# Kernel tuning notes

Hardware: AMD Instinct MI355X
Metric: run time of the kernel (lower is better)

Reference implementation:

```python
import jax, jax.numpy as jnp
import numpy as np

B, S, D, H = 4, 2048, 1024, 16
DK = D // H
THETA = 10000.0


def setup_inputs() -> dict:
    key = jax.random.key(0)
    ks = jax.random.split(key, 5)
    std = (1.0 / D) ** 0.5
    return {
        "x": jax.random.normal(ks[0], (B, S, D), dtype=jnp.float32),
        "q_proj": jax.random.normal(ks[1], (D, D), dtype=jnp.float32) * std,
        "k_proj": jax.random.normal(ks[2], (D, D), dtype=jnp.float32) * std,
        "v_proj": jax.random.normal(ks[3], (D, D), dtype=jnp.float32) * std,
        "o_proj": jax.random.normal(ks[4], (D, D), dtype=jnp.float32) * std,
        "token_positions": jnp.broadcast_to(jnp.arange(S, dtype=jnp.int32), (B, S)),
    }


def _apply_rope(t, cos, sin):
    # t: (B,H,S,DK); cos/sin: (B,1,S,DK//2). Interleaved even/odd rotation.
    even = t[..., 0::2]
    odd = t[..., 1::2]
    r_even = even * cos - odd * sin
    r_odd = even * sin + odd * cos
    return jnp.stack([r_even, r_odd], axis=-1).reshape(t.shape)


def reference(x, q_proj, k_proj, v_proj, o_proj, token_positions):
    b, s, d = x.shape
    # QKV projections: weights stored (out, in) -> x @ W^T
    q = (x @ q_proj.T).reshape(b, s, H, DK).transpose(0, 2, 1, 3)  # (B,H,S,DK)
    k = (x @ k_proj.T).reshape(b, s, H, DK).transpose(0, 2, 1, 3)
    v = (x @ v_proj.T).reshape(b, s, H, DK).transpose(0, 2, 1, 3)

    # RoPE angles from token positions
    inv_freq = 1.0 / (THETA ** (jnp.arange(0, DK, 2, dtype=jnp.float32) / DK))  # (DK/2,)
    ang = token_positions.astype(jnp.float32)[..., None] * inv_freq  # (B,S,DK/2)
    cos = jnp.cos(ang)[:, None, :, :]  # (B,1,S,DK/2)
    sin = jnp.sin(ang)[:, None, :, :]
    q = _apply_rope(q, cos, sin)
    k = _apply_rope(k, cos, sin)

    # Full causal attention with explicit score matrix (faithful to source)
    scores = jnp.einsum("bhqd,bhkd->bhqk", q, k) / (DK ** 0.5)
    causal = jnp.tril(jnp.ones((s, s), dtype=bool))
    scores = jnp.where(causal, scores, -jnp.inf)
    attn = jax.nn.softmax(scores, axis=-1)
    out = jnp.einsum("bhqk,bhkd->bhqd", attn, v)  # (B,H,S,DK)
    out = out.transpose(0, 2, 1, 3).reshape(b, s, d)  # (B,S,D)
    # o_proj stored (d_out, d_model): out @ o_proj^T
    return out @ o_proj.T
```

## Files before the change

### kernel.cpp

```cpp
#include <hip/hip_runtime.h>
#include <hip/hip_bf16.h>

using bf16x8 = __attribute__((ext_vector_type(8))) short;
using f32x4  = __attribute__((ext_vector_type(4))) float;

#define MFMA_BF16(a, b, c) __builtin_amdgcn_mfma_f32_16x16x32_bf16((a), (b), (c), 0, 0, 0)

__device__ __forceinline__ unsigned short f2bf(float x) {
  union { float f; unsigned int u; } v; v.f = x;
  unsigned int r = v.u + 0x7fffu + ((v.u >> 16) & 1u);
  return (unsigned short)(r >> 16);
}

__device__ __forceinline__ unsigned int cvtpk(float a, float b) {
  __hip_bfloat162 h = __float22bfloat162_rn(make_float2(a, b));
  unsigned int u; __builtin_memcpy(&u, &h, 4); return u;
}

__device__ __forceinline__ unsigned int pack_trunc(float a, float b) {
  unsigned int ua, ub;
  __builtin_memcpy(&ua, &a, 4);
  __builtin_memcpy(&ub, &b, 4);
  return (ua >> 16) | (ub & 0xFFFF0000u);
}

__device__ __forceinline__ float fast_exp2(float x) {
#if __has_builtin(__builtin_amdgcn_exp2f)
  return __builtin_amdgcn_exp2f(x);
#else
  return exp2f(x);
#endif
}

__device__ __forceinline__ void gload16(const void* g, void* l) {
  __builtin_amdgcn_global_load_lds(
      (const __attribute__((address_space(1))) unsigned int*)g,
      (__attribute__((address_space(3))) unsigned int*)l, 16, 0, 0);
}

__device__ __forceinline__ void wait_and_barrier() {
  asm volatile("s_waitcnt vmcnt(0)" ::: "memory");
  __builtin_amdgcn_sched_barrier(0);
  __builtin_amdgcn_s_barrier();
  __builtin_amdgcn_sched_barrier(0);
}

__global__ __launch_bounds__(256) void cvt_all(const float* __restrict__ x,
                                               const float* __restrict__ qw,
                                               const float* __restrict__ kw,
                                               const float* __restrict__ vw,
                                               const float* __restrict__ ow,
                                               unsigned short* __restrict__ out) {
  const int bid = blockIdx.x;
  int seg, loc;
  if (bid < 8192) { seg = 0; loc = bid; }
  else { seg = 1 + ((bid - 8192) >> 10); loc = (bid - 8192) & 1023; }
  const float* srcs[5] = {x, qw, kw, vw, ow};
  const float* in = srcs[seg];
  const size_t obase = (seg == 0) ? 0 : ((size_t)8192 + (size_t)(seg - 1) * 1024) * 1024;
  const int i = loc * 1024 + threadIdx.x * 4;
  float4 f = *(const float4*)(in + i);
  ushort4 o;
  o.x = f2bf(f.x); o.y = f2bf(f.y); o.z = f2bf(f.z); o.w = f2bf(f.w);
  *(ushort4*)(out + obase + i) = o;
}

__global__ __launch_bounds__(256) void rope_tab_k(const int* __restrict__ pos,
                                                  float2* __restrict__ tab) {
  const int row = blockIdx.x * 8 + (threadIdx.x >> 5);
  const int i = threadIdx.x & 31;
  const float p = (float)pos[row];
  const float invf = exp2f((float)(2 * i) * (-13.287712379549609f / 64.0f));
  float sn, cs;
  sincosf(p * invf, &sn, &cs);
  tab[(size_t)row * 32 + i] = make_float2(cs, sn);
}

template <int MODE>
__global__ __launch_bounds__(256) void gemm_bt(const unsigned short* __restrict__ A,
                                               const unsigned short* __restrict__ Bw,
                                               void* __restrict__ outp,
                                               const float2* __restrict__ tab,
                                               float oscale) {
  constexpr int K = 1024;
  __shared__ __align__(16) unsigned short smem[12288];
  const int tid  = threadIdx.x;
  const int lane = tid & 63, wave = tid >> 6;
  const int wr = wave >> 1, wc = wave & 1;
  const int bid = blockIdx.x + (blockIdx.y << 3);
  const int xcd = bid & 7;
  const int t6  = bid >> 3;
  const int bn0 = (t6 & 7) * 128;
  const int bm0 = (((t6 >> 3) << 3) + xcd) * 64;
  const int lrow = lane & 15, hi = lane >> 4, lko = hi * 8;
  const int srow = tid >> 2, scol = (tid & 3) * 8;
  const unsigned short* gA = A + (size_t)(bm0 + srow) * K + scol;
  const unsigned short* gB = Bw + (size_t)(bn0 + srow) * K + scol;
  const f32x4 z = {0.f, 0.f, 0.f, 0.f};
  f32x4 acc[2][4];
#pragma unroll
  for (int i = 0; i < 2; ++i)
#pragma unroll
    for (int j = 0; j < 4; ++j) acc[i][j] = z;

  auto stage = [&](int k0, int c) {
    char* base = (char*)smem + c * 12288;
    gload16(gA + k0, base + wave * 1024);
    gload16(gB + k0, base + 4096 + wave * 1024);
    gload16(gB + k0 + (size_t)64 * K, base + 8192 + wave * 1024);
  };

  stage(0, 0);
  int cur = 0;
#pragma unroll 1
  for (int k0 = 0; k0 < K; k0 += 32) {
    wait_and_barrier();
    if (k0 + 32 < K) stage(k0 + 32, cur ^ 1);
    const int ub = cur * 6144;
    bf16x8 af[2], bfr[4];
#pragma unroll
    for (int mi = 0; mi < 2; ++mi)
      af[mi] = *(const bf16x8*)&smem[ub + (wr * 32 + mi * 16 + lrow) * 32 + lko];
#pragma unroll
    for (int ni = 0; ni < 4; ++ni)
      bfr[ni] = *(const bf16x8*)&smem[ub + 2048 + (wc * 64 + ni * 16 + lrow) * 32 + lko];
#pragma unroll
    for (int mi = 0; mi < 2; ++mi)
#pragma unroll
      for (int ni = 0; ni < 4; ++ni)
        acc[mi][ni] = MFMA_BF16(af[mi], bfr[ni], acc[mi][ni]);
    cur ^= 1;
  }

  if (MODE == 2) {
#pragma unroll
    for (int mi = 0; mi < 2; ++mi)
#pragma unroll
      for (int r = 0; r < 4; ++r) {
        const int row = bm0 + wr * 32 + mi * 16 + hi * 4 + r;
#pragma unroll
        for (int ni = 0; ni < 4; ++ni) {
          const int col = bn0 + wc * 64 + ni * 16 + lrow;
          ((float*)outp)[(size_t)row * 1024 + col] = acc[mi][ni][r];
        }
      }
    return;
  }

  const int h0 = bn0 >> 6;
  const int bb = bm0 >> 11, s0 = bm0 & 2047;
  unsigned short* dst = (unsigned short*)outp;
  __syncthreads();
  if (MODE == 0) {
#pragma unroll
    for (int mi = 0; mi < 2; ++mi)
#pragma unroll
      for (int ni = 0; ni < 4; ++ni) {
        const int col = wc * 64 + ni * 16 + lrow;
        const int d = col & 63;
#pragma unroll
        for (int r = 0; r < 4; ++r) {
          const int row = wr * 32 + mi * 16 + hi * 4 + r;
          const float2 t = tab[(size_t)(bm0 + row) * 32 + (d >> 1)];
          const float v = acc[mi][ni][r];
          const float other = __shfl_xor(v, 1);
          const float rv = (d & 1) ? (other * t.y + v * t.x) : (v * t.x - other * t.y);
          smem[row * 136 + col] = f2bf(rv * oscale);
        }
      }
    __syncthreads();
#pragma unroll
    for (int it = 0; it < 4; ++it) {
      const int c = it * 256 + tid;
      const int hl = c >> 9, rem = c & 511;
      const int sl = rem >> 3, ch = (rem & 7) * 8;
      const bf16x8 val = *(const bf16x8*)&smem[sl * 136 + hl * 64 + ch];
      *(bf16x8*)&dst[((size_t)(bb * 16 + h0 + hl) * 2048 + s0 + sl) * 64 + ch] = val;
    }
  } else {
#pragma unroll
    for (int mi = 0; mi < 2; ++mi)
#pragma unroll
      for (int ni = 0; ni < 4; ++ni) {
        const int col = wc * 64 + ni * 16 + lrow;
        ushort4 pk;
        pk.x = f2bf(acc[mi][ni][0]); pk.y = f2bf(acc[mi][ni][1]);
        pk.z = f2bf(acc[mi][ni][2]); pk.w = f2bf(acc[mi][ni][3]);
        *(ushort4*)&smem[col * 72 + wr * 32 + mi * 16 + hi * 4] = pk;
      }
    __syncthreads();
#pragma unroll
    for (int it = 0; it < 4; ++it) {
      const int c = it * 256 + tid;
      const int cl = c >> 3, sc = (c & 7) * 8;
      const bf16x8 val = *(const bf16x8*)&smem[cl * 72 + sc];
      *(bf16x8*)&dst[((size_t)(bb * 16 + h0 + (cl >> 6)) * 64 + (cl & 63)) * 2048 + s0 + sc] = val;
    }
  }
}

__global__ __launch_bounds__(256) void attn_fwd(const unsigned short* __restrict__ Q,
                                                const unsigned short* __restrict__ Kk,
                                                const unsigned short* __restrict__ Vt,
                                                unsigned short* __restrict__ O) {
  __shared__ __align__(16) unsigned short Ks[8192];
  __shared__ __align__(16) unsigned short Vs[8192];
  __shared__ __align__(16) unsigned short Plds[4][16][64];
  const int p = blockIdx.x;
  const int L = (p & 7) * 128 + (p >> 3);
  const int bh = L >> 4, pair = L & 15;
  const int tid = threadIdx.x;
  const int lane = tid & 63, wave = tid >> 6;
  const int lrow = lane & 15, hi = lane >> 4;
  const int l7 = lrow & 7;
  const unsigned short* Qb = Q + (size_t)bh * 2048 * 64;
  const unsigned short* Kb = Kk + (size_t)bh * 2048 * 64;
  const unsigned short* Vb = Vt + (size_t)bh * 64 * 2048;
  const int rK   = tid >> 3;
  const int colK = ((tid & 7) ^ ((tid >> 3) & 7)) * 8;
  const int rV   = tid >> 4;
  const int colV = ((tid & 8) | ((tid & 7) ^ ((tid >> 4) & 7))) * 8;
  const int b = bh >> 4, h = bh & 15;
  const f32x4 z = {0.f, 0.f, 0.f, 0.f};
  const short one = (short)0x3F80;
  const bf16x8 ones = {one, one, one, one, one, one, one, one};

  auto stage128 = [&](int kv0) {
#pragma unroll
    for (int pass = 0; pass < 4; ++pass)
      gload16(Kb + (size_t)(kv0 + rK + 32 * pass) * 64 + colK,
              (char*)Ks + pass * 4096 + wave * 1024);
#pragma unroll
    for (int pass = 0; pass < 4; ++pass)
      gload16(Vb + (size_t)(rV + 16 * pass) * 2048 + kv0 + colV,
              (char*)Vs + pass * 4096 + wave * 1024);
  };
  auto stage64 = [&](int kv0) {
#pragma unroll
    for (int pass = 0; pass < 2; ++pass)
      gload16(Kb + (size_t)(kv0 + rK + 32 * pass) * 64 + colK,
              (char*)Ks + pass * 4096 + wave * 1024);
#pragma unroll
    for (int pass = 0; pass < 2; ++pass)
      gload16(Vb + (size_t)(rK + 32 * pass) * 2048 + kv0 + colK,
              (char*)Vs + pass * 4096 + wave * 1024);
  };

  for (int half = 0; half < 2; ++half) {
    const int qb = half ? (31 - pair) : pair;
    const int qrow = qb * 64 + wave * 16;
    const int qg = qrow + lrow;
    const bf16x8 qf0 = *(const bf16x8*)(Qb + (size_t)qg * 64 + hi * 8);
    const bf16x8 qf1 = *(const bf16x8*)(Qb + (size_t)qg * 64 + 32 + hi * 8);
    f32x4 acc[4] = {z, z, z, z};
    f32x4 acc_l = z;

    auto compute64 = [&](const char* Kbase, const char* Vbase, int vstride,
                         int kv0g, bool diag) {
      f32x4 st[4];
      __builtin_amdgcn_s_setprio(1);
#pragma unroll
      for (int n = 0; n < 4; ++n) {
        const int rk = n * 16 + lrow;
        const bf16x8 kf0 = *(const bf16x8*)(Kbase + rk * 128 + ((hi ^ l7) * 16));
        const bf16x8 kf1 = *(const bf16x8*)(Kbase + rk * 128 + (((4 + hi) ^ l7) * 16));
        st[n] = MFMA_BF16(kf0, qf0, z);
        st[n] = MFMA_BF16(kf1, qf1, st[n]);
      }
      __builtin_amdgcn_s_setprio(0);
      if (diag) {
#pragma unroll
        for (int n = 0; n < 4; ++n)
#pragma unroll
          for (int r = 0; r < 4; ++r)
            if (kv0g + n * 16 + hi * 4 + r > qg) st[n][r] = -1e30f;
      }
      float pe[16];
#pragma unroll
      for (int n = 0; n < 4; ++n)
#pragma unroll
        for (int r = 0; r < 4; ++r) pe[n * 4 + r] = fast_exp2(st[n][r]);
#pragma unroll
      for (int n = 0; n < 4; ++n) {
        uint2 pk;
        pk.x = pack_trunc(pe[n * 4 + 0], pe[n * 4 + 1]);
        pk.y = pack_trunc(pe[n * 4 + 2], pe[n * 4 + 3]);
        const int eo = ((((n * 2 + (hi >> 1)) ^ l7) << 3) | ((hi & 1) << 2));
        *(uint2*)&Plds[wave][lrow][eo] = pk;
      }
      const bf16x8 pf0 = *(const bf16x8*)&Plds[wave][lrow][(hi ^ l7) << 3];
      const bf16x8 pf1 = *(const bf16x8*)&Plds[wave][lrow][((4 + hi) ^ l7) << 3];
      __builtin_amdgcn_s_setprio(1);
      acc_l = MFMA_BF16(ones, pf0, acc_l);
      acc_l = MFMA_BF16(ones, pf1, acc_l);
#pragma unroll
      for (int dt = 0; dt < 4; ++dt) {
        const int rv = dt * 16 + lrow;
        const bf16x8 vf0 = *(const bf16x8*)(Vbase + rv * vstride + ((hi ^ l7) * 16));
        const bf16x8 vf1 = *(const bf16x8*)(Vbase + rv * vstride + (((4 + hi) ^ l7) * 16));
        acc[dt] = MFMA_BF16(vf0, pf0, acc[dt]);
        acc[dt] = MFMA_BF16(vf1, pf1, acc[dt]);
      }
      __builtin_amdgcn_s_setprio(0);
    };

    const int F = (qb + 1) >> 1;
    const bool tail = ((qb & 1) == 0);
#pragma unroll 1
    for (int f = 0; f < F; ++f) {
      const int kv0 = f * 128;
      __syncthreads();
      stage128(kv0);
      __syncthreads();
      compute64((char*)Ks, (char*)Vs, 256, kv0, false);
      compute64((char*)Ks + 8192, (char*)Vs + 128, 256, kv0 + 64,
                (f == F - 1) && !tail);
    }
    if (tail) {
      const int kv0 = qb * 64;
      __syncthreads();
      stage64(kv0);
      __syncthreads();
      compute64((char*)Ks, (char*)Vs, 128, kv0, true);
    }

    const float inv = 1.0f / acc_l[0];
#pragma unroll
    for (int dt = 0; dt < 4; ++dt) {
      uint2 ov;
      ov.x = cvtpk(acc[dt][0] * inv, acc[dt][1] * inv);
      ov.y = cvtpk(acc[dt][2] * inv, acc[dt][3] * inv);
      *(uint2*)&O[((size_t)b * 2048 + qg) * 1024 + h * 64 + dt * 16 + hi * 4] = ov;
    }
  }
}

extern "C" void kernel_launch(void* const* d_in, const int* in_sizes, int n_in,
                              void* d_out, int out_size, void* d_ws, size_t ws_size,
                              hipStream_t stream) {
  const float* x  = (const float*)d_in[0];
  const float* qw = (const float*)d_in[1];
  const float* kw = (const float*)d_in[2];
  const float* vw = (const float*)d_in[3];
  const float* ow = (const float*)d_in[4];
  const int* pos  = (const int*)d_in[5];
  float* out = (float*)d_out;

  unsigned short* xb  = (unsigned short*)d_ws;
  unsigned short* qwb = xb  + (size_t)8192 * 1024;
  unsigned short* kwb = qwb + (size_t)1024 * 1024;
  unsigned short* vwb = kwb + (size_t)1024 * 1024;
  unsigned short* owb = vwb + (size_t)1024 * 1024;
  unsigned short* Qr  = owb + (size_t)1024 * 1024;
  unsigned short* Kr  = Qr  + (size_t)8192 * 1024;
  unsigned short* Vtr = Kr  + (size_t)8192 * 1024;
  unsigned short* AO  = Vtr + (size_t)8192 * 1024;
  float2* tab = (float2*)(AO + (size_t)8192 * 1024);

  cvt_all<<<12288, 256, 0, stream>>>(x, qw, kw, vw, ow, xb);
  rope_tab_k<<<1024, 256, 0, stream>>>(pos, tab);

  constexpr float SCALE = 0.18033688011112042f;
  dim3 gg(8, 128);
  gemm_bt<0><<<gg, 256, 0, stream>>>(xb, qwb, Qr,  tab, SCALE);
  gemm_bt<0><<<gg, 256, 0, stream>>>(xb, kwb, Kr,  tab, 1.0f);
  gemm_bt<1><<<gg, 256, 0, stream>>>(xb, vwb, Vtr, nullptr, 1.0f);
  attn_fwd<<<1024, 256, 0, stream>>>(Qr, Kr, Vtr, AO);
  gemm_bt<2><<<gg, 256, 0, stream>>>(AO, owb, out, nullptr, 1.0f);
}
```

Before: 181.8 us.

## Process two 64-row query blocks per wave to reuse K/V tiles

The attention kernel now gives each workgroup 128 query rows, as two 64-row sub-blocks per wave, instead of 64. Each staged 128-key K/V tile and its register fragments serve both sub-blocks, which halves the K/V global and LDS traffic per query. The grid drops from 1024 to 512 blocks, the separate 64-key tail stage is removed, and diagonal masking moves to the first and second halves of the tile. The cost is higher register pressure (two accumulator sets, K and V fragments held in registers) and fewer blocks for load balancing.

```diff
diff --git a/kernel.cpp b/kernel.cpp
--- a/kernel.cpp
+++ b/kernel.cpp
@@ -207,8 +207,8 @@
   __shared__ __align__(16) unsigned short Vs[8192];
   __shared__ __align__(16) unsigned short Plds[4][16][64];
   const int p = blockIdx.x;
-  const int L = (p & 7) * 128 + (p >> 3);
-  const int bh = L >> 4, pair = L & 15;
+  const int L = (p & 7) * 64 + (p >> 3);
+  const int bh = L >> 3, pr = L & 7;
   const int tid = threadIdx.x;
   const int lane = tid & 63, wave = tid >> 6;
   const int lrow = lane & 15, hi = lane >> 4;
@@ -224,6 +224,7 @@
   const f32x4 z = {0.f, 0.f, 0.f, 0.f};
   const short one = (short)0x3F80;
   const bf16x8 ones = {one, one, one, one, one, one, one, one};
+  const int qrl = wave * 16 + lrow;
 
   auto stage128 = [&](int kv0) {
 #pragma unroll
@@ -235,45 +236,26 @@
       gload16(Vb + (size_t)(rV + 16 * pass) * 2048 + kv0 + colV,
               (char*)Vs + pass * 4096 + wave * 1024);
   };
-  auto stage64 = [&](int kv0) {
-#pragma unroll
-    for (int pass = 0; pass < 2; ++pass)
-      gload16(Kb + (size_t)(kv0 + rK + 32 * pass) * 64 + colK,
-              (char*)Ks + pass * 4096 + wave * 1024);
-#pragma unroll
-    for (int pass = 0; pass < 2; ++pass)
-      gload16(Vb + (size_t)(rK + 32 * pass) * 2048 + kv0 + colK,
-              (char*)Vs + pass * 4096 + wave * 1024);
-  };
 
   for (int half = 0; half < 2; ++half) {
-    const int qb = half ? (31 - pair) : pair;
-    const int qrow = qb * 64 + wave * 16;
-    const int qg = qrow + lrow;
-    const bf16x8 qf0 = *(const bf16x8*)(Qb + (size_t)qg * 64 + hi * 8);
-    const bf16x8 qf1 = *(const bf16x8*)(Qb + (size_t)qg * 64 + 32 + hi * 8);
-    f32x4 acc[4] = {z, z, z, z};
-    f32x4 acc_l = z;
-
-    auto compute64 = [&](const char* Kbase, const char* Vbase, int vstride,
-                         int kv0g, bool diag) {
-      f32x4 st[4];
-      __builtin_amdgcn_s_setprio(1);
-#pragma unroll
-      for (int n = 0; n < 4; ++n) {
-        const int rk = n * 16 + lrow;
-        const bf16x8 kf0 = *(const bf16x8*)(Kbase + rk * 128 + ((hi ^ l7) * 16));
-        const bf16x8 kf1 = *(const bf16x8*)(Kbase + rk * 128 + (((4 + hi) ^ l7) * 16));
-        st[n] = MFMA_BF16(kf0, qf0, z);
-        st[n] = MFMA_BF16(kf1, qf1, st[n]);
-      }
-      __builtin_amdgcn_s_setprio(0);
-      if (diag) {
+    const int qb = half ? (15 - pr) : pr;
+    const int qga = qb * 128 + qrl;
+    const int qgb = qga + 64;
+    const bf16x8 qfa0 = *(const bf16x8*)(Qb + (size_t)qga * 64 + hi * 8);
+    const bf16x8 qfa1 = *(const bf16x8*)(Qb + (size_t)qga * 64 + 32 + hi * 8);
+    const bf16x8 qfb0 = *(const bf16x8*)(Qb + (size_t)qgb * 64 + hi * 8);
+    const bf16x8 qfb1 = *(const bf16x8*)(Qb + (size_t)qgb * 64 + 32 + hi * 8);
+    f32x4 acca[4] = {z, z, z, z}, accb[4] = {z, z, z, z};
+    f32x4 acc_la = z, acc_lb = z;
+
+    auto sm_pv = [&](f32x4* st, const bf16x8* vf, f32x4* acc, f32x4& acc_l,
+                     bool dg) {
+      if (dg) {
 #pragma unroll
         for (int n = 0; n < 4; ++n)
 #pragma unroll
           for (int r = 0; r < 4; ++r)
-            if (kv0g + n * 16 + hi * 4 + r > qg) st[n][r] = -1e30f;
+            if (n * 16 + hi * 4 + r > qrl) st[n][r] = -1e30f;
       }
       float pe[16];
 #pragma unroll
@@ -290,47 +272,72 @@
       }
       const bf16x8 pf0 = *(const bf16x8*)&Plds[wave][lrow][(hi ^ l7) << 3];
       const bf16x8 pf1 = *(const bf16x8*)&Plds[wave][lrow][((4 + hi) ^ l7) << 3];
-      __builtin_amdgcn_s_setprio(1);
       acc_l = MFMA_BF16(ones, pf0, acc_l);
       acc_l = MFMA_BF16(ones, pf1, acc_l);
 #pragma unroll
       for (int dt = 0; dt < 4; ++dt) {
+        acc[dt] = MFMA_BF16(vf[dt * 2], pf0, acc[dt]);
+        acc[dt] = MFMA_BF16(vf[dt * 2 + 1], pf1, acc[dt]);
+      }
+    };
+
+    auto process_half = [&](const char* Kbase, const char* Vbase,
+                            bool doA, bool dgA, bool dgB) {
+      bf16x8 kf[8];
+#pragma unroll
+      for (int n = 0; n < 4; ++n) {
+        const int rk = n * 16 + lrow;
+        kf[n * 2]     = *(const bf16x8*)(Kbase + rk * 128 + ((hi ^ l7) * 16));
+        kf[n * 2 + 1] = *(const bf16x8*)(Kbase + rk * 128 + (((4 + hi) ^ l7) * 16));
+      }
+      f32x4 sta[4], stb[4];
+      __builtin_amdgcn_s_setprio(1);
+      if (doA) {
+#pragma unroll
+        for (int n = 0; n < 4; ++n) {
+          sta[n] = MFMA_BF16(kf[n * 2], qfa0, z);
+          sta[n] = MFMA_BF16(kf[n * 2 + 1], qfa1, sta[n]);
+        }
+      }
+#pragma unroll
+      for (int n = 0; n < 4; ++n) {
+        stb[n] = MFMA_BF16(kf[n * 2], qfb0, z);
+        stb[n] = MFMA_BF16(kf[n * 2 + 1], qfb1, stb[n]);
+      }
+      __builtin_amdgcn_s_setprio(0);
+      bf16x8 vf[8];
+#pragma unroll
+      for (int dt = 0; dt < 4; ++dt) {
         const int rv = dt * 16 + lrow;
-        const bf16x8 vf0 = *(const bf16x8*)(Vbase + rv * vstride + ((hi ^ l7) * 16));
-        const bf16x8 vf1 = *(const bf16x8*)(Vbase + rv * vstride + (((4 + hi) ^ l7) * 16));
-        acc[dt] = MFMA_BF16(vf0, pf0, acc[dt]);
-        acc[dt] = MFMA_BF16(vf1, pf1, acc[dt]);
-      }
-      __builtin_amdgcn_s_setprio(0);
+        vf[dt * 2]     = *(const bf16x8*)(Vbase + rv * 256 + ((hi ^ l7) * 16));
+        vf[dt * 2 + 1] = *(const bf16x8*)(Vbase + rv * 256 + (((4 + hi) ^ l7) * 16));
+      }
+      if (doA) sm_pv(sta, vf, acca, acc_la, dgA);
+      sm_pv(stb, vf, accb, acc_lb, dgB);
     };
 
-    const int F = (qb + 1) >> 1;
-    const bool tail = ((qb & 1) == 0);
 #pragma unroll 1
-    for (int f = 0; f < F; ++f) {
-      const int kv0 = f * 128;
+    for (int f = 0; f <= qb; ++f) {
       __syncthreads();
-      stage128(kv0);
+      stage128(f * 128);
       __syncthreads();
-      compute64((char*)Ks, (char*)Vs, 256, kv0, false);
-      compute64((char*)Ks + 8192, (char*)Vs + 128, 256, kv0 + 64,
-                (f == F - 1) && !tail);
+      const bool dg = (f == qb);
+      process_half((char*)Ks, (char*)Vs, true, dg, false);
+      process_half((char*)Ks + 8192, (char*)Vs + 128, !dg, false, dg);
     }
-    if (tail) {
-      const int kv0 = qb * 64;
-      __syncthreads();
-      stage64(kv0);
-      __syncthreads();
-      compute64((char*)Ks, (char*)Vs, 128, kv0, true);
-    }
-
-    const float inv = 1.0f / acc_l[0];
+
+    const float inva = 1.0f / acc_la[0];
+    const float invb = 1.0f / acc_lb[0];
 #pragma unroll
     for (int dt = 0; dt < 4; ++dt) {
       uint2 ov;
-      ov.x = cvtpk(acc[dt][0] * inv, acc[dt][1] * inv);
-      ov.y = cvtpk(acc[dt][2] * inv, acc[dt][3] * inv);
-      *(uint2*)&O[((size_t)b * 2048 + qg) * 1024 + h * 64 + dt * 16 + hi * 4] = ov;
+      ov.x = cvtpk(acca[dt][0] * inva, acca[dt][1] * inva);
+      ov.y = cvtpk(acca[dt][2] * inva, acca[dt][3] * inva);
+      *(uint2*)&O[((size_t)b * 2048 + qga) * 1024 + h * 64 + dt * 16 + hi * 4] = ov;
+      uint2 ow2;
+      ow2.x = cvtpk(accb[dt][0] * invb, accb[dt][1] * invb);
+      ow2.y = cvtpk(accb[dt][2] * invb, accb[dt][3] * invb);
+      *(uint2*)&O[((size_t)b * 2048 + qgb) * 1024 + h * 64 + dt * 16 + hi * 4] = ow2;
     }
   }
 }
@@ -365,6 +372,6 @@
   gemm_bt<0><<<gg, 256, 0, stream>>>(xb, qwb, Qr,  tab, SCALE);
   gemm_bt<0><<<gg, 256, 0, stream>>>(xb, kwb, Kr,  tab, 1.0f);
   gemm_bt<1><<<gg, 256, 0, stream>>>(xb, vwb, Vtr, nullptr, 1.0f);
-  attn_fwd<<<1024, 256, 0, stream>>>(Qr, Kr, Vtr, AO);
+  attn_fwd<<<512, 256, 0, stream>>>(Qr, Kr, Vtr, AO);
   gemm_bt<2><<<gg, 256, 0, stream>>>(AO, owb, out, nullptr, 1.0f);
 }
```

Result: faster. 177.9 us (-2.1%).
